# Optimization experiments

Hardware: AMD Instinct MI355X
Metric: run time of the kernel (lower is better)

Reference implementation:

```python
import jax, jax.numpy as jnp
import numpy as np

TEMPERATURE = 10.0
N_CLASSES = 10


def _sqdist(a, b):
    # squared euclidean distances, [Na, Nb] == torch.cdist(a, b) ** 2
    an = jnp.sum(a * a, axis=1)[:, None]
    bn = jnp.sum(b * b, axis=1)[None, :]
    return jnp.maximum(an + bn - 2.0 * (a @ b.T), 0.0)


def setup_inputs() -> dict:
    key = jax.random.key(0)
    ks = jax.random.split(key, 6)
    B, N, D, H, C = 512, 4096, 512, 2048, N_CLASSES
    return {
        "x": jax.random.normal(ks[0], (B, D), dtype=jnp.float32),
        "star_features": jax.random.normal(ks[1], (N, D), dtype=jnp.float32),
        "from_features": jax.random.normal(ks[2], (N, D), dtype=jnp.float32),
        "star_label_ids": jax.random.randint(ks[3], (N,), 0, C),
        "W1": jax.random.normal(ks[4], (D, H), dtype=jnp.float32) * 0.02,
        "b1": jnp.zeros((H,), dtype=jnp.float32),
        "W2": jax.random.normal(ks[5], (H, C), dtype=jnp.float32) * 0.02,
        "b2": jnp.zeros((C,), dtype=jnp.float32),
    }


def _transport_features(x, feats_to, star_feats):
    # dists: [N_star, B]
    d = _sqdist(star_feats, x)
    d = d / jnp.mean(d, axis=0, keepdims=True)
    e = jnp.exp(-TEMPERATURE * d)                    # [N_star, B]
    w = feats_to.T @ e                               # [d_to, B]
    return (w / jnp.sum(e, axis=0, keepdims=True)).T  # [B, d_to]


def reference(x, star_features, from_features, star_label_ids, W1, b1, W2, b2):
    B = x.shape[0]
    C = N_CLASSES
    # --- exact-match lookup against dataset_star features (fused eq+all reduce) ---
    mask = jnp.all(x[:, None, :] == star_features[None, :, :], axis=2)  # [B, N_star]
    matched = jnp.any(mask, axis=1)                                      # [B]
    match_idx = jnp.argmax(mask, axis=1)                                 # [B]
    # --- transport features: matched samples take aligned dataset sample, rest use OT map ---
    xt_unmatched = _transport_features(x, from_features, star_features)  # [B, d]
    xt_matched = from_features[match_idx]                                # [B, d]
    x_transported = jnp.where(matched[:, None], xt_matched, xt_unmatched)
    # --- run the model in the transported domain (MLP classifier) ---
    h = jax.nn.relu(x_transported @ W1 + b1)
    logits = h @ W2 + b2                                                 # [B, C]
    # --- project_labels: preds and one-hot unique labels have equal dim -> cdist/argmin branch ---
    unique_labels = jnp.eye(C, dtype=logits.dtype)
    closest = jnp.argmin(_sqdist(logits, unique_labels), axis=1)
    y_proj = unique_labels[closest]                                      # [B, C] (unused by 'all_features')
    # --- transport_labels, method='all_features': feature-distance-weighted average of star labels ---
    d2 = _sqdist(from_features, x_transported)                           # [N_from, B]
    d2 = d2 / jnp.mean(d2, axis=0, keepdims=True)
    e2 = jnp.exp(-TEMPERATURE * d2)
    star_labels = jax.nn.one_hot(star_label_ids, C, dtype=x.dtype)       # [N_star, C]
    y_star = (star_labels.T @ e2 / jnp.sum(e2, axis=0, keepdims=True)).T  # [B, C]
    # single (model, dataset) pair -> sum/len is identity
    return y_star
```

## Files before the change

### kernel.cpp

```cpp
#include <hip/hip_runtime.h>

#define TEMP 10.0f
#define NS 4096
#define BB 512
#define DDIM 512
#define NCLS 10
#define LDSP 72

typedef short bf16x8 __attribute__((ext_vector_type(8)));
typedef float f32x4 __attribute__((ext_vector_type(4)));

__device__ inline short f2bf(float f) {
    unsigned u = __builtin_bit_cast(unsigned, f);
    u += 0x7FFFu + ((u >> 16) & 1u);
    return (short)(u >> 16);
}
__device__ inline float bf2f(short h) {
    unsigned u = ((unsigned)(unsigned short)h) << 16;
    return __builtin_bit_cast(float, u);
}

__device__ inline float block_sum(float s, float* red) {
    #pragma unroll
    for (int off = 32; off > 0; off >>= 1) s += __shfl_down(s, off);
    int wid = threadIdx.x >> 6;
    if ((threadIdx.x & 63) == 0) red[wid] = s;
    __syncthreads();
    float tot = red[0] + red[1] + red[2] + red[3];
    __syncthreads();
    return tot;
}

__global__ __launch_bounds__(256)
void prep(const float* __restrict__ x, const float* __restrict__ star,
          const float* __restrict__ from,
          short* __restrict__ Xb, short* __restrict__ Sb,
          short* __restrict__ FTb, short* __restrict__ Fb,
          float* __restrict__ xn2, float* __restrict__ sn2, float* __restrict__ fn2,
          float* __restrict__ scol, float* __restrict__ xcol, int* __restrict__ midx,
          float* __restrict__ spart, float* __restrict__ fpart)
{
    int bid = blockIdx.x, t = threadIdx.x;
    if (bid < 2176) {
        const float* in; short* outb; float* n2; float* colb; int rowbase;
        if (bid < 1024)      { in = star; outb = Sb; n2 = sn2; colb = scol; rowbase = bid * 4; }
        else if (bid < 1152) { in = x;    outb = Xb; n2 = xn2; colb = xcol; rowbase = (bid - 1024) * 4; }
        else                 { in = from; outb = Fb; n2 = fn2; colb = nullptr; rowbase = (bid - 1152) * 4; }
        if (bid == 1024) { midx[t] = NS; midx[256 + t] = NS; }
        int row = rowbase + (t >> 6);
        int l = t & 63;
        const float4* p = (const float4*)(in + (size_t)row * DDIM) + l * 2;
        float4 a = p[0], b = p[1];
        float s = a.x*a.x + a.y*a.y + a.z*a.z + a.w*a.w
                + b.x*b.x + b.y*b.y + b.z*b.z + b.w*b.w;
        bf16x8 h;
        h[0]=f2bf(a.x); h[1]=f2bf(a.y); h[2]=f2bf(a.z); h[3]=f2bf(a.w);
        h[4]=f2bf(b.x); h[5]=f2bf(b.y); h[6]=f2bf(b.z); h[7]=f2bf(b.w);
        *(bf16x8*)(outb + (size_t)row * DDIM + l * 8) = h;
        #pragma unroll
        for (int off = 32; off > 0; off >>= 1) s += __shfl_down(s, off);
        if (l == 0) {
            n2[row] = s;
            if (colb) colb[row] = a.x;
        }
        return;
    }
    if (bid >= 2688) {
        __shared__ float cp[512];
        int ib = bid - 2688;
        const float* M = (ib < 128) ? star : from;
        float* part = (ib < 128) ? spart : fpart;
        int r0 = (ib & 127) * 32;
        int c4 = (t & 127) * 4, rg = t >> 7;
        float4 acc = {0.f, 0.f, 0.f, 0.f};
        #pragma unroll 4
        for (int r = rg; r < 32; r += 2) {
            float4 v = *(const float4*)(M + (size_t)(r0 + r) * DDIM + c4);
            acc.x += v.x; acc.y += v.y; acc.z += v.z; acc.w += v.w;
        }
        if (rg == 1) *(float4*)&cp[c4] = acc;
        __syncthreads();
        if (rg == 0) {
            float4 o = *(const float4*)&cp[c4];
            acc.x += o.x; acc.y += o.y; acc.z += o.z; acc.w += o.w;
            *(float4*)&part[(size_t)(ib & 127) * 512 + c4] = acc;
        }
        return;
    }
    __shared__ short tile[64][LDSP];
    int tid2 = bid - 2176;
    int n0 = (tid2 & 63) * 64, d0 = (tid2 >> 6) * 64;
    int r = t >> 4, c4 = (t & 15) * 4;
    #pragma unroll
    for (int rr = 0; rr < 64; rr += 16) {
        float4 v = *(const float4*)(from + (size_t)(n0 + r + rr) * DDIM + d0 + c4);
        tile[r + rr][c4 + 0] = f2bf(v.x);
        tile[r + rr][c4 + 1] = f2bf(v.y);
        tile[r + rr][c4 + 2] = f2bf(v.z);
        tile[r + rr][c4 + 3] = f2bf(v.w);
    }
    __syncthreads();
    int dr = t >> 2, nco = (t & 3) * 16;
    short tmp[16];
    #pragma unroll
    for (int q = 0; q < 16; ++q) tmp[q] = tile[nco + q][dr];
    short* op = FTb + (size_t)(d0 + dr) * NS + n0 + nco;
    *(bf16x8*)op       = *(bf16x8*)tmp;
    *(bf16x8*)(op + 8) = *(bf16x8*)(tmp + 8);
}

__global__ __launch_bounds__(256)
void finmeans(const float* __restrict__ spart, const float* __restrict__ fpart,
              const float* __restrict__ sn2, const float* __restrict__ fn2,
              float* __restrict__ sbar, float* __restrict__ fbar,
              float* __restrict__ sms, float* __restrict__ fms)
{
    __shared__ float red[4];
    int bid = blockIdx.x, t = threadIdx.x;
    const float* part = bid ? fpart : spart;
    const float* n2v  = bid ? fn2 : sn2;
    float* outm = bid ? fbar : sbar;
    float* outs = bid ? fms : sms;
    float ax = 0.f, ay = 0.f;
    #pragma unroll 8
    for (int k = 0; k < 128; ++k) {
        float2 v = *(const float2*)(part + (size_t)k * 512 + t * 2);
        ax += v.x; ay += v.y;
    }
    float2 o; o.x = ax * (1.0f / NS); o.y = ay * (1.0f / NS);
    *(float2*)(outm + t * 2) = o;
    float s = 0.f;
    #pragma unroll
    for (int q = 0; q < 16; ++q) s += n2v[q * 256 + t];
    float tot = block_sum(s, red);
    if (t == 0) outs[0] = tot * (1.0f / NS);
}

__global__ __launch_bounds__(256)
void aux(const float* __restrict__ x, const float* __restrict__ star,
         const float* __restrict__ sbar, const float* __restrict__ sms,
         const float* __restrict__ xn2, float* __restrict__ escale1,
         const float* __restrict__ scol, const float* __restrict__ xcol,
         int* __restrict__ midx)
{
    int bid = blockIdx.x, t = threadIdx.x;
    if (bid < 128) {
        int lane = t & 63, w = t >> 6;
        int b = bid * 4 + w;
        const float4* xp = (const float4*)(x + (size_t)b * DDIM) + lane * 2;
        const float4* sp = (const float4*)sbar + lane * 2;
        float4 xa = xp[0], xb = xp[1], sa = sp[0], sb = sp[1];
        float dot = xa.x*sa.x + xa.y*sa.y + xa.z*sa.z + xa.w*sa.w
                  + xb.x*sb.x + xb.y*sb.y + xb.z*sb.z + xb.w*sb.w;
        #pragma unroll
        for (int m = 32; m > 0; m >>= 1) dot += __shfl_xor(dot, m);
        if (lane == 0)
            escale1[b] = -TEMP / (sms[0] + xn2[b] - 2.0f * dot);
        return;
    }
    __shared__ float xl[BB];
    *(float2*)&xl[t * 2] = *(const float2*)&xcol[t * 2];
    __syncthreads();
    int n = (bid - 128) * 256 + t;
    float sv = scol[n];
    #pragma unroll 4
    for (int b4 = 0; b4 < BB; b4 += 4) {
        float4 xv = *(const float4*)&xl[b4];
        if (xv.x == sv || xv.y == sv || xv.z == sv || xv.w == sv) {
            #pragma unroll
            for (int j = 0; j < 4; ++j) {
                int b = b4 + j;
                if (xl[b] == sv) {
                    const float* xr = x + (size_t)b * DDIM;
                    const float* sr = star + (size_t)n * DDIM;
                    bool eq = true;
                    for (int k = 0; k < DDIM && eq; k += 4) {
                        float4 a = *(const float4*)(xr + k);
                        float4 c = *(const float4*)(sr + k);
                        eq = (a.x == c.x) && (a.y == c.y) &&
                             (a.z == c.z) && (a.w == c.w);
                    }
                    if (eq) atomicMin(&midx[b], n);
                }
            }
        }
    }
}

template<int WSE>
__global__ __launch_bounds__(512)
void gemm_exp(const short* __restrict__ A, const short* __restrict__ B,
              const float* __restrict__ an2, const float* __restrict__ bn2,
              const float* __restrict__ escale, short* __restrict__ Eout,
              float* __restrict__ sumEp)
{
    __shared__ short As[2][64][LDSP];
    __shared__ short Bs[2][128][LDSP];
    __shared__ float se[4][64];
    const int K = DDIM;
    int t = threadIdx.x;
    int m0 = blockIdx.x * 64;
    int n0 = blockIdx.y * 128;
    int wid = t >> 6, lane = t & 63;
    int wr = wid >> 2, wc = wid & 3;
    int lr = lane & 15, lk = lane >> 4;

    int ar = t >> 3, ak = (t & 7) * 8;
    int br = t >> 2, bk = (t & 3) * 16;
    const short* Ag = A + (size_t)(m0 + ar) * K + ak;
    const short* Bg = B + (size_t)(n0 + br) * K + bk;

    f32x4 acc[2][2] = {};
    bf16x8 ra0 = *(const bf16x8*)Ag;
    bf16x8 rb0 = *(const bf16x8*)Bg;
    bf16x8 rb1 = *(const bf16x8*)(Bg + 8);
    int cur = 0;
    *(bf16x8*)&As[0][ar][ak]     = ra0;
    *(bf16x8*)&Bs[0][br][bk]     = rb0;
    *(bf16x8*)&Bs[0][br][bk + 8] = rb1;

    const int nt = K / 64;
    for (int it = 0; it < nt; ++it) {
        __syncthreads();
        if (it + 1 < nt) {
            int ko = (it + 1) * 64;
            ra0 = *(const bf16x8*)(Ag + ko);
            rb0 = *(const bf16x8*)(Bg + ko);
            rb1 = *(const bf16x8*)(Bg + ko + 8);
        }
        #pragma unroll
        for (int ks = 0; ks < 2; ++ks) {
            int k0 = ks * 32 + lk * 8;
            bf16x8 af[2], bfr[2];
            #pragma unroll
            for (int i = 0; i < 2; ++i)
                af[i] = *(const bf16x8*)&As[cur][wr * 32 + i * 16 + lr][k0];
            #pragma unroll
            for (int j = 0; j < 2; ++j)
                bfr[j] = *(const bf16x8*)&Bs[cur][wc * 32 + j * 16 + lr][k0];
            #pragma unroll
            for (int i = 0; i < 2; ++i)
                #pragma unroll
                for (int j = 0; j < 2; ++j)
                    acc[i][j] = __builtin_amdgcn_mfma_f32_16x16x32_bf16(
                        af[i], bfr[j], acc[i][j], 0, 0, 0);
        }
        if (it + 1 < nt) {
            cur ^= 1;
            *(bf16x8*)&As[cur][ar][ak]     = ra0;
            *(bf16x8*)&Bs[cur][br][bk]     = rb0;
            *(bf16x8*)&Bs[cur][br][bk + 8] = rb1;
        }
    }
    float bn2v[2];
    int gnv[2];
    #pragma unroll
    for (int j = 0; j < 2; ++j) { gnv[j] = n0 + wc * 32 + j * 16 + lr; bn2v[j] = bn2[gnv[j]]; }
    #pragma unroll
    for (int i = 0; i < 2; ++i) {
        #pragma unroll
        for (int r = 0; r < 4; ++r) {
            int gm = m0 + wr * 32 + i * 16 + lk * 4 + r;
            float a2 = an2[gm];
            float sc = escale[gm];
            float rs = 0.f;
            #pragma unroll
            for (int j = 0; j < 2; ++j) {
                float dv = fmaxf(a2 + bn2v[j] - 2.0f * acc[i][j][r], 0.0f);
                short hb = f2bf(__expf(dv * sc));
                Eout[(size_t)gm * NS + gnv[j]] = hb;
                if (WSE) rs += bf2f(hb);
            }
            if (WSE) {
                #pragma unroll
                for (int m = 1; m < 16; m <<= 1) rs += __shfl_xor(rs, m);
                if (lr == 0) se[wc][wr * 32 + i * 16 + lk * 4 + r] = rs;
            }
        }
    }
    if (WSE) {
        __syncthreads();
        if (t < 64)
            sumEp[(size_t)(m0 + t) * 32 + blockIdx.y] =
                se[0][t] + se[1][t] + se[2][t] + se[3][t];
    }
}

__global__ __launch_bounds__(512)
void gemm_bt8(const short* __restrict__ A, const short* __restrict__ B, int K,
              int kslab, int nt, float* __restrict__ C, int ldc, size_t cstride)
{
    __shared__ short As[2][64][LDSP];
    __shared__ short Bs[2][128][LDSP];
    int t = threadIdx.x;
    int m0 = blockIdx.x * 64;
    int n0 = blockIdx.y * 128;
    int kbase = blockIdx.z * kslab;
    float* Cp = C + (size_t)blockIdx.z * cstride;
    int wid = t >> 6, lane = t & 63;
    int wr = wid >> 2, wc = wid & 3;
    int lr = lane & 15, lk = lane >> 4;

    int ar = t >> 3, ak = (t & 7) * 8;
    int br = t >> 2, bk = (t & 3) * 16;
    const short* Ag = A + (size_t)(m0 + ar) * K + kbase + ak;
    const short* Bg = B + (size_t)(n0 + br) * K + kbase + bk;

    f32x4 acc[2][2] = {};
    bf16x8 ra0 = *(const bf16x8*)Ag;
    bf16x8 rb0 = *(const bf16x8*)Bg;
    bf16x8 rb1 = *(const bf16x8*)(Bg + 8);
    int cur = 0;
    *(bf16x8*)&As[0][ar][ak]     = ra0;
    *(bf16x8*)&Bs[0][br][bk]     = rb0;
    *(bf16x8*)&Bs[0][br][bk + 8] = rb1;

    for (int it = 0; it < nt; ++it) {
        __syncthreads();
        if (it + 1 < nt) {
            int ko = (it + 1) * 64;
            ra0 = *(const bf16x8*)(Ag + ko);
            rb0 = *(const bf16x8*)(Bg + ko);
            rb1 = *(const bf16x8*)(Bg + ko + 8);
        }
        #pragma unroll
        for (int ks = 0; ks < 2; ++ks) {
            int k0 = ks * 32 + lk * 8;
            bf16x8 af[2], bfr[2];
            #pragma unroll
            for (int i = 0; i < 2; ++i)
                af[i] = *(const bf16x8*)&As[cur][wr * 32 + i * 16 + lr][k0];
            #pragma unroll
            for (int j = 0; j < 2; ++j)
                bfr[j] = *(const bf16x8*)&Bs[cur][wc * 32 + j * 16 + lr][k0];
            #pragma unroll
            for (int i = 0; i < 2; ++i)
                #pragma unroll
                for (int j = 0; j < 2; ++j)
                    acc[i][j] = __builtin_amdgcn_mfma_f32_16x16x32_bf16(
                        af[i], bfr[j], acc[i][j], 0, 0, 0);
        }
        if (it + 1 < nt) {
            cur ^= 1;
            *(bf16x8*)&As[cur][ar][ak]     = ra0;
            *(bf16x8*)&Bs[cur][br][bk]     = rb0;
            *(bf16x8*)&Bs[cur][br][bk + 8] = rb1;
        }
    }
    #pragma unroll
    for (int i = 0; i < 2; ++i) {
        #pragma unroll
        for (int r = 0; r < 4; ++r) {
            int gm = m0 + wr * 32 + i * 16 + lk * 4 + r;
            #pragma unroll
            for (int j = 0; j < 2; ++j) {
                int gn = n0 + wc * 32 + j * 16 + lr;
                Cp[(size_t)gm * ldc + gn] = acc[i][j][r];
            }
        }
    }
}

__global__ __launch_bounds__(256)
void xt_fin(const float* __restrict__ wpart, const float* __restrict__ sumEp,
            const int* __restrict__ midx, const float* __restrict__ fromf,
            const float* __restrict__ fbar, const float* __restrict__ fms,
            short* __restrict__ xtb, float* __restrict__ xtn2,
            float* __restrict__ escale2)
{
    __shared__ float red[4];
    __shared__ float bc[1];
    int b = blockIdx.x;
    int t = threadIdx.x;
    int d = t * 2;
    int mi = midx[b];
    if (t == 0) {
        float s = 0.f;
        #pragma unroll
        for (int k = 0; k < 32; ++k) s += sumEp[(size_t)b * 32 + k];
        bc[0] = 1.0f / s;
    }
    float v0 = 0.f, v1 = 0.f;
    #pragma unroll
    for (int sl = 0; sl < 8; ++sl) {
        float2 p = *(const float2*)(wpart + (size_t)sl * (BB * DDIM) + (size_t)b * DDIM + d);
        v0 += p.x; v1 += p.y;
    }
    __syncthreads();
    float inv = bc[0];
    v0 *= inv; v1 *= inv;
    if (mi < NS) {
        v0 = fromf[(size_t)mi * DDIM + d];
        v1 = fromf[(size_t)mi * DDIM + d + 1];
    }
    xtb[(size_t)b * DDIM + d]     = f2bf(v0);
    xtb[(size_t)b * DDIM + d + 1] = f2bf(v1);
    float nt2 = block_sum(v0 * v0 + v1 * v1, red);
    float2 fb2 = *(const float2*)(fbar + d);
    float fd = block_sum(v0 * fb2.x + v1 * fb2.y, red);
    if (t == 0) {
        xtn2[b] = nt2;
        escale2[b] = -TEMP / (fms[0] + nt2 - 2.0f * fd);
    }
}

__global__ __launch_bounds__(256)
void ystar_fin(const short* __restrict__ e2T, const int* __restrict__ labels,
               float* __restrict__ out)
{
    __shared__ float cred[NCLS + 1][4];
    int b = blockIdx.x;
    int t = threadIdx.x;
    const short* row = e2T + (size_t)b * NS + t * 16;
    bf16x8 h0 = *(const bf16x8*)row;
    bf16x8 h1 = *(const bf16x8*)(row + 8);
    float accs[NCLS] = {};
    float te = 0.f;
    #pragma unroll
    for (int q = 0; q < 4; ++q) {
        int4 lb = *(const int4*)(labels + t * 16 + q * 4);
        int lbl[4] = {lb.x, lb.y, lb.z, lb.w};
        #pragma unroll
        for (int e = 0; e < 4; ++e) {
            int idx = q * 4 + e;
            float ev = bf2f(idx < 8 ? h0[idx] : h1[idx - 8]);
            te += ev;
            #pragma unroll
            for (int c = 0; c < NCLS; ++c) accs[c] += (lbl[e] == c) ? ev : 0.f;
        }
    }
    int wid = t >> 6, lane = t & 63;
    #pragma unroll
    for (int c = 0; c < NCLS + 1; ++c) {
        float sv = (c < NCLS) ? accs[c] : te;
        #pragma unroll
        for (int off = 32; off > 0; off >>= 1) sv += __shfl_down(sv, off);
        if (lane == 0) cred[c][wid] = sv;
    }
    __syncthreads();
    if (t < NCLS) {
        float num = cred[t][0] + cred[t][1] + cred[t][2] + cred[t][3];
        float den = cred[NCLS][0] + cred[NCLS][1] + cred[NCLS][2] + cred[NCLS][3];
        out[b * NCLS + t] = num / den;
    }
}

extern "C" void kernel_launch(void* const* d_in, const int* in_sizes, int n_in,
                              void* d_out, int out_size, void* d_ws, size_t ws_size,
                              hipStream_t stream) {
    const float* x     = (const float*)d_in[0];
    const float* star  = (const float*)d_in[1];
    const float* from  = (const float*)d_in[2];
    const int*   label = (const int*)d_in[3];
    float* out = (float*)d_out;

    float* F = (float*)d_ws;
    float* wpart = F;
    short* Sb    = (short*)(F + 4194304);
    short* FTb   = (short*)(F + 5242880);
    short* Fb    = (short*)(F + 6291456);
    short* Eb    = (short*)(F + 7340032);
    short* E2b   = (short*)(F + 8388608);
    short* Xb    = (short*)(F + 9437184);
    short* XTb   = (short*)(F + 9568256);
    float* sn2   = F + 9699328;
    float* fn2   = F + 9703424;
    float* xn2   = F + 9707520;
    float* xtn2  = F + 9708032;
    float* esc1  = F + 9708544;
    float* esc2  = F + 9709056;
    float* sbar  = F + 9709568;
    float* fbar  = F + 9710080;
    float* sms   = F + 9710592;
    float* fms   = F + 9710608;
    float* sumEp = F + 9710624;
    float* scol  = F + 9727008;
    float* xcol  = F + 9731104;
    int*   midx  = (int*)(F + 9731616);
    float* spart = F + 9732128;
    float* fpart = F + 9797664;

    prep<<<2944, 256, 0, stream>>>(x, star, from, Xb, Sb, FTb, Fb,
                                   xn2, sn2, fn2, scol, xcol, midx, spart, fpart);
    finmeans<<<2, 256, 0, stream>>>(spart, fpart, sn2, fn2, sbar, fbar, sms, fms);
    aux<<<144, 256, 0, stream>>>(x, star, sbar, sms, xn2, esc1, scol, xcol, midx);
    gemm_exp<1><<<dim3(8, 32), 512, 0, stream>>>(Xb, Sb, xn2, sn2, esc1, Eb, sumEp);
    gemm_bt8<<<dim3(8, 4, 8), 512, 0, stream>>>(Eb, FTb, NS, 512, 8, wpart, DDIM,
                                                (size_t)BB * DDIM);
    xt_fin<<<BB, 256, 0, stream>>>(wpart, sumEp, midx, from, fbar, fms,
                                   XTb, xtn2, esc2);
    gemm_exp<0><<<dim3(8, 32), 512, 0, stream>>>(XTb, Fb, xtn2, fn2, esc2, E2b, nullptr);
    ystar_fin<<<BB, 256, 0, stream>>>(E2b, label, out);
}
```

Before: 79.43 us.

## Fuse column-sum partials into row prep and shrink gemm_exp tiles to 64x64

The separate column-sum blocks in prep are removed. Each row-conversion block now writes its own per-4-row column partial through LDS, which finmeans reduces over 1024 partials instead of 128. This saves a second read of star and from, but finmeans does 8x more serial loads. gemm_exp moves from 64x128 tiles with 512 threads to 64x64 tiles with 256 threads, doubling the grid to 512 blocks for better CU occupancy. The sumEp layout grows to 64 partials per row, and xt_fin now sums them with a block reduction.

```diff
diff --git a/kernel.cpp b/kernel.cpp
--- a/kernel.cpp
+++ b/kernel.cpp
@@ -40,14 +40,19 @@
           float* __restrict__ scol, float* __restrict__ xcol, int* __restrict__ midx,
           float* __restrict__ spart, float* __restrict__ fpart)
 {
+    __shared__ short tile[64][LDSP];
     int bid = blockIdx.x, t = threadIdx.x;
     if (bid < 2176) {
-        const float* in; short* outb; float* n2; float* colb; int rowbase;
-        if (bid < 1024)      { in = star; outb = Sb; n2 = sn2; colb = scol; rowbase = bid * 4; }
-        else if (bid < 1152) { in = x;    outb = Xb; n2 = xn2; colb = xcol; rowbase = (bid - 1024) * 4; }
-        else                 { in = from; outb = Fb; n2 = fn2; colb = nullptr; rowbase = (bid - 1152) * 4; }
+        const float* in; short* outb; float* n2; float* colb; float* part; int rowbase;
+        if (bid < 1024)      { in = star; outb = Sb; n2 = sn2; colb = scol; rowbase = bid * 4;
+                               part = spart + (size_t)bid * 512; }
+        else if (bid < 1152) { in = x;    outb = Xb; n2 = xn2; colb = xcol; rowbase = (bid - 1024) * 4;
+                               part = nullptr; }
+        else                 { in = from; outb = Fb; n2 = fn2; colb = nullptr; rowbase = (bid - 1152) * 4;
+                               part = fpart + (size_t)(bid - 1152) * 512; }
         if (bid == 1024) { midx[t] = NS; midx[256 + t] = NS; }
-        int row = rowbase + (t >> 6);
+        int w = t >> 6;
+        int row = rowbase + w;
         int l = t & 63;
         const float4* p = (const float4*)(in + (size_t)row * DDIM) + l * 2;
         float4 a = p[0], b = p[1];
@@ -63,31 +68,19 @@
             n2[row] = s;
             if (colb) colb[row] = a.x;
         }
+        if (part) {
+            float* cp = (float*)tile;
+            *(float4*)&cp[w * 512 + l * 8]     = a;
+            *(float4*)&cp[w * 512 + l * 8 + 4] = b;
+            __syncthreads();
+            int c = t * 2;
+            float2 o;
+            o.x = cp[c]       + cp[512 + c]     + cp[1024 + c]     + cp[1536 + c];
+            o.y = cp[c + 1]   + cp[512 + c + 1] + cp[1024 + c + 1] + cp[1536 + c + 1];
+            *(float2*)&part[c] = o;
+        }
         return;
     }
-    if (bid >= 2688) {
-        __shared__ float cp[512];
-        int ib = bid - 2688;
-        const float* M = (ib < 128) ? star : from;
-        float* part = (ib < 128) ? spart : fpart;
-        int r0 = (ib & 127) * 32;
-        int c4 = (t & 127) * 4, rg = t >> 7;
-        float4 acc = {0.f, 0.f, 0.f, 0.f};
-        #pragma unroll 4
-        for (int r = rg; r < 32; r += 2) {
-            float4 v = *(const float4*)(M + (size_t)(r0 + r) * DDIM + c4);
-            acc.x += v.x; acc.y += v.y; acc.z += v.z; acc.w += v.w;
-        }
-        if (rg == 1) *(float4*)&cp[c4] = acc;
-        __syncthreads();
-        if (rg == 0) {
-            float4 o = *(const float4*)&cp[c4];
-            acc.x += o.x; acc.y += o.y; acc.z += o.z; acc.w += o.w;
-            *(float4*)&part[(size_t)(ib & 127) * 512 + c4] = acc;
-        }
-        return;
-    }
-    __shared__ short tile[64][LDSP];
     int tid2 = bid - 2176;
     int n0 = (tid2 & 63) * 64, d0 = (tid2 >> 6) * 64;
     int r = t >> 4, c4 = (t & 15) * 4;
@@ -123,7 +116,7 @@
     float* outs = bid ? fms : sms;
     float ax = 0.f, ay = 0.f;
     #pragma unroll 8
-    for (int k = 0; k < 128; ++k) {
+    for (int k = 0; k < 1024; ++k) {
         float2 v = *(const float2*)(part + (size_t)k * 512 + t * 2);
         ax += v.x; ay += v.y;
     }
@@ -188,43 +181,44 @@
 }
 
 template<int WSE>
-__global__ __launch_bounds__(512)
+__global__ __launch_bounds__(256)
 void gemm_exp(const short* __restrict__ A, const short* __restrict__ B,
               const float* __restrict__ an2, const float* __restrict__ bn2,
               const float* __restrict__ escale, short* __restrict__ Eout,
-              float* __restrict__ sumEp)
+              float* __restrict__ sumEp, int nt)
 {
     __shared__ short As[2][64][LDSP];
-    __shared__ short Bs[2][128][LDSP];
-    __shared__ float se[4][64];
+    __shared__ short Bs[2][64][LDSP];
+    __shared__ float se[2][64];
     const int K = DDIM;
     int t = threadIdx.x;
     int m0 = blockIdx.x * 64;
-    int n0 = blockIdx.y * 128;
+    int n0 = blockIdx.y * 64;
     int wid = t >> 6, lane = t & 63;
-    int wr = wid >> 2, wc = wid & 3;
+    int wr = wid >> 1, wc = wid & 1;
     int lr = lane & 15, lk = lane >> 4;
 
-    int ar = t >> 3, ak = (t & 7) * 8;
-    int br = t >> 2, bk = (t & 3) * 16;
+    int ar = t >> 2, ak = (t & 3) * 16;
     const short* Ag = A + (size_t)(m0 + ar) * K + ak;
-    const short* Bg = B + (size_t)(n0 + br) * K + bk;
+    const short* Bg = B + (size_t)(n0 + ar) * K + ak;
 
     f32x4 acc[2][2] = {};
     bf16x8 ra0 = *(const bf16x8*)Ag;
+    bf16x8 ra1 = *(const bf16x8*)(Ag + 8);
     bf16x8 rb0 = *(const bf16x8*)Bg;
     bf16x8 rb1 = *(const bf16x8*)(Bg + 8);
     int cur = 0;
     *(bf16x8*)&As[0][ar][ak]     = ra0;
-    *(bf16x8*)&Bs[0][br][bk]     = rb0;
-    *(bf16x8*)&Bs[0][br][bk + 8] = rb1;
-
-    const int nt = K / 64;
+    *(bf16x8*)&As[0][ar][ak + 8] = ra1;
+    *(bf16x8*)&Bs[0][ar][ak]     = rb0;
+    *(bf16x8*)&Bs[0][ar][ak + 8] = rb1;
+
     for (int it = 0; it < nt; ++it) {
         __syncthreads();
         if (it + 1 < nt) {
             int ko = (it + 1) * 64;
             ra0 = *(const bf16x8*)(Ag + ko);
+            ra1 = *(const bf16x8*)(Ag + ko + 8);
             rb0 = *(const bf16x8*)(Bg + ko);
             rb1 = *(const bf16x8*)(Bg + ko + 8);
         }
@@ -248,8 +242,9 @@
         if (it + 1 < nt) {
             cur ^= 1;
             *(bf16x8*)&As[cur][ar][ak]     = ra0;
-            *(bf16x8*)&Bs[cur][br][bk]     = rb0;
-            *(bf16x8*)&Bs[cur][br][bk + 8] = rb1;
+            *(bf16x8*)&As[cur][ar][ak + 8] = ra1;
+            *(bf16x8*)&Bs[cur][ar][ak]     = rb0;
+            *(bf16x8*)&Bs[cur][ar][ak + 8] = rb1;
         }
     }
     float bn2v[2];
@@ -281,8 +276,7 @@
     if (WSE) {
         __syncthreads();
         if (t < 64)
-            sumEp[(size_t)(m0 + t) * 32 + blockIdx.y] =
-                se[0][t] + se[1][t] + se[2][t] + se[3][t];
+            sumEp[(size_t)(m0 + t) * 64 + blockIdx.y] = se[0][t] + se[1][t];
     }
 }
 
@@ -369,25 +363,19 @@
             float* __restrict__ escale2)
 {
     __shared__ float red[4];
-    __shared__ float bc[1];
     int b = blockIdx.x;
     int t = threadIdx.x;
     int d = t * 2;
     int mi = midx[b];
-    if (t == 0) {
-        float s = 0.f;
-        #pragma unroll
-        for (int k = 0; k < 32; ++k) s += sumEp[(size_t)b * 32 + k];
-        bc[0] = 1.0f / s;
-    }
+    float sv = (t < 64) ? sumEp[(size_t)b * 64 + t] : 0.f;
+    float stot = block_sum(sv, red);
+    float inv = 1.0f / stot;
     float v0 = 0.f, v1 = 0.f;
     #pragma unroll
     for (int sl = 0; sl < 8; ++sl) {
         float2 p = *(const float2*)(wpart + (size_t)sl * (BB * DDIM) + (size_t)b * DDIM + d);
         v0 += p.x; v1 += p.y;
     }
-    __syncthreads();
-    float inv = bc[0];
     v0 *= inv; v1 *= inv;
     if (mi < NS) {
         v0 = fromf[(size_t)mi * DDIM + d];
@@ -456,39 +444,39 @@
 
     float* F = (float*)d_ws;
     float* wpart = F;
-    short* Sb    = (short*)(F + 4194304);
-    short* FTb   = (short*)(F + 5242880);
-    short* Fb    = (short*)(F + 6291456);
-    short* Eb    = (short*)(F + 7340032);
-    short* E2b   = (short*)(F + 8388608);
-    short* Xb    = (short*)(F + 9437184);
-    short* XTb   = (short*)(F + 9568256);
-    float* sn2   = F + 9699328;
-    float* fn2   = F + 9703424;
-    float* xn2   = F + 9707520;
-    float* xtn2  = F + 9708032;
-    float* esc1  = F + 9708544;
-    float* esc2  = F + 9709056;
-    float* sbar  = F + 9709568;
-    float* fbar  = F + 9710080;
-    float* sms   = F + 9710592;
-    float* fms   = F + 9710608;
-    float* sumEp = F + 9710624;
-    float* scol  = F + 9727008;
-    float* xcol  = F + 9731104;
-    int*   midx  = (int*)(F + 9731616);
-    float* spart = F + 9732128;
-    float* fpart = F + 9797664;
-
-    prep<<<2944, 256, 0, stream>>>(x, star, from, Xb, Sb, FTb, Fb,
+    short* Sb    = (short*)(F + 2097152);
+    short* FTb   = (short*)(F + 3145728);
+    short* Fb    = (short*)(F + 4194304);
+    short* Eb    = (short*)(F + 5242880);
+    short* E2b   = (short*)(F + 6291456);
+    short* Xb    = (short*)(F + 7340032);
+    short* XTb   = (short*)(F + 7471104);
+    float* sn2   = F + 7602176;
+    float* fn2   = F + 7606272;
+    float* xn2   = F + 7610368;
+    float* xtn2  = F + 7610880;
+    float* esc1  = F + 7611392;
+    float* esc2  = F + 7611904;
+    float* sbar  = F + 7612416;
+    float* fbar  = F + 7612928;
+    float* sms   = F + 7613440;
+    float* fms   = F + 7613456;
+    float* sumEp = F + 7613472;
+    float* scol  = F + 7646240;
+    float* xcol  = F + 7650336;
+    int*   midx  = (int*)(F + 7650848);
+    float* spart = F + 7651360;
+    float* fpart = F + 8175648;
+
+    prep<<<2688, 256, 0, stream>>>(x, star, from, Xb, Sb, FTb, Fb,
                                    xn2, sn2, fn2, scol, xcol, midx, spart, fpart);
     finmeans<<<2, 256, 0, stream>>>(spart, fpart, sn2, fn2, sbar, fbar, sms, fms);
     aux<<<144, 256, 0, stream>>>(x, star, sbar, sms, xn2, esc1, scol, xcol, midx);
-    gemm_exp<1><<<dim3(8, 32), 512, 0, stream>>>(Xb, Sb, xn2, sn2, esc1, Eb, sumEp);
+    gemm_exp<1><<<dim3(8, 64), 256, 0, stream>>>(Xb, Sb, xn2, sn2, esc1, Eb, sumEp, 8);
     gemm_bt8<<<dim3(8, 4, 8), 512, 0, stream>>>(Eb, FTb, NS, 512, 8, wpart, DDIM,
                                                 (size_t)BB * DDIM);
     xt_fin<<<BB, 256, 0, stream>>>(wpart, sumEp, midx, from, fbar, fms,
                                    XTb, xtn2, esc2);
-    gemm_exp<0><<<dim3(8, 32), 512, 0, stream>>>(XTb, Fb, xtn2, fn2, esc2, E2b, nullptr);
+    gemm_exp<0><<<dim3(8, 64), 256, 0, stream>>>(XTb, Fb, xtn2, fn2, esc2, E2b, nullptr, 8);
     ystar_fin<<<BB, 256, 0, stream>>>(E2b, label, out);
 }
```

After: 117.7 us. +48.2%, slower.
